# Optimization experiments

Hardware: AMD Instinct MI355X
Metric: run time of the kernel (lower is better)

Reference implementation:

```python
import jax, jax.numpy as jnp
import numpy as np

N = 8192
HID = 64
TAU = 0.8
LAMBDA = 0.5
POS_DENSITY = 0.005


def setup_inputs() -> dict:
    key = jax.random.key(0)
    k1, k2, k3, k4, k5, k6, k7 = jax.random.split(key, 7)
    x1 = jax.random.normal(k1, (N, HID), dtype=jnp.float32)
    x2 = jax.random.normal(k2, (N, HID), dtype=jnp.float32)
    # xavier_uniform with gain=1.414 for square [HID, HID] linears
    limit = 1.414 * np.sqrt(6.0 / (HID + HID))
    W1 = jax.random.uniform(k3, (HID, HID), dtype=jnp.float32, minval=-limit, maxval=limit)
    b1 = jnp.zeros((HID,), dtype=jnp.float32)
    W2 = jax.random.uniform(k4, (HID, HID), dtype=jnp.float32, minval=-limit, maxval=limit)
    b2 = jnp.zeros((HID,), dtype=jnp.float32)
    pm = (jax.random.uniform(k5, (N, N), dtype=jnp.float32) < POS_DENSITY).astype(jnp.float32)
    positive_matrix = jnp.maximum(pm, jnp.eye(N, dtype=jnp.float32))
    return {"x1": x1, "x2": x2, "W1": W1, "b1": b1, "W2": W2, "b2": b2,
            "positive_matrix": positive_matrix}


def _project(x, W1, b1, W2, b2):
    # nn.Linear(hidden, hidden) -> ELU -> nn.Linear(hidden, hidden)
    h = jax.nn.elu(x @ W1.T + b1)
    return h @ W2.T + b2


def _l2norm(z, eps=1e-12):
    # F.normalize(p=2, dim=1): x / max(||x||, eps)
    n = jnp.linalg.norm(z, axis=-1, keepdims=True)
    return z / jnp.maximum(n, eps)


def _sim(z1, z2, tau):
    return jnp.exp((_l2norm(z1) @ _l2norm(z2).T) / tau)  # [N, N]


def _masked_loss(sim_mat, pos):
    row = sim_mat / (jnp.sum(sim_mat, axis=-1, keepdims=True) + 1e-8)
    return -jnp.log(jnp.sum(row * pos, axis=-1) + 1e-8).mean()


def reference(x1, x2, W1, b1, W2, b2, positive_matrix):
    z1 = _project(x1, W1, b1, W2, b2)
    z2 = _project(x2, W1, b1, W2, b2)
    sc_mp = _sim(z1, z2, TAU)
    mp_sc = _sim(z2, z1, TAU)
    sc_loss = _masked_loss(sc_mp, positive_matrix)
    mp_loss = _masked_loss(mp_sc, positive_matrix)
    return sc_loss * LAMBDA + mp_loss * (1.0 - LAMBDA)
```

## Files before the change

### kernel.cpp

```cpp
#include <hip/hip_runtime.h>
#include <hip/hip_bf16.h>

#define N 8192
#define HID 64

typedef __attribute__((ext_vector_type(4))) float f32x4;
typedef __attribute__((ext_vector_type(8))) __bf16 bf16x8;

#if __has_builtin(__builtin_amdgcn_exp2f)
__device__ __forceinline__ float fast_exp2(float x) {
  return __builtin_amdgcn_exp2f(x);
}
#else
__device__ __forceinline__ float fast_exp2(float x) {
  float r;
  asm volatile("v_exp_f32 %0, %1" : "=v"(r) : "v"(x));
  return r;
}
#endif

__device__ __forceinline__ f32x4 nt_load4(const float* p) {
  return __builtin_nontemporal_load((const f32x4*)p);
}

__device__ __forceinline__ void gload_lds16(const void* g, float* l) {
  __builtin_amdgcn_global_load_lds(
      (const __attribute__((address_space(1))) void*)g,
      (__attribute__((address_space(3))) void*)l, 16, 0, 0);
}

__global__ __launch_bounds__(256) void proj_kernel(
    const float* __restrict__ x1, const float* __restrict__ x2,
    const float* __restrict__ W1, const float* __restrict__ b1,
    const float* __restrict__ W2, const float* __restrict__ b2,
    __bf16* __restrict__ Z1h, __bf16* __restrict__ Z2h)
{
  __shared__ __align__(16) float w1s[64*68];
  __shared__ __align__(16) float w2s[64*68];
  __shared__ __align__(16) float xs[4][64];
  __shared__ __align__(16) float hs[4][64];

  const int tid  = threadIdx.x;
  const int lane = tid & 63;
  const int w    = tid >> 6;

  for (int idx = tid; idx < 64*64; idx += 256) {
    int j = idx >> 6, k = idx & 63;
    w1s[j*68+k] = W1[idx];
    w2s[j*68+k] = W2[idx];
  }
  __syncthreads();

  const float bias1 = b1[lane];
  const float bias2 = b2[lane];

  const int wave_global = blockIdx.x * 4 + w;
  #pragma unroll 1
  for (int it = 0; it < 4; ++it) {
    int R = wave_global * 4 + it;
    const float* src; __bf16* dst;
    if (R < N) { src = x1 + (size_t)R*HID;      dst = Z1h + (size_t)R*HID; }
    else       { src = x2 + (size_t)(R-N)*HID;  dst = Z2h + (size_t)(R-N)*HID; }

    float xv = src[lane];
    xs[w][lane] = xv;
    float acc = bias1;
    #pragma unroll
    for (int qq = 0; qq < 16; ++qq) {
      f32x4 xq = *(const f32x4*)&xs[w][qq*4];
      f32x4 wq = *(const f32x4*)&w1s[lane*68 + qq*4];
      acc += xq.x*wq.x + xq.y*wq.y + xq.z*wq.z + xq.w*wq.w;
    }
    float h = acc > 0.f ? acc : expm1f(acc);
    hs[w][lane] = h;
    float acc2 = bias2;
    #pragma unroll
    for (int qq = 0; qq < 16; ++qq) {
      f32x4 hq = *(const f32x4*)&hs[w][qq*4];
      f32x4 wq = *(const f32x4*)&w2s[lane*68 + qq*4];
      acc2 += hq.x*wq.x + hq.y*wq.y + hq.z*wq.z + hq.w*wq.w;
    }
    float z = acc2;
    float ss = z*z;
    #pragma unroll
    for (int m = 1; m < 64; m <<= 1) ss += __shfl_xor(ss, m);
    float inv = 1.0f / fmaxf(sqrtf(ss), 1e-12f);
    dst[lane] = (__bf16)(z * inv);
  }
}

__global__ __launch_bounds__(256, 4) void sim_kernel(
    const __bf16* __restrict__ Z1h, const __bf16* __restrict__ Z2h,
    const float* __restrict__ pos,
    float* __restrict__ pr1, float* __restrict__ pn1,
    float* __restrict__ pr2, float* __restrict__ pn2)
{
  __shared__ __align__(16) float zs1[128*32];
  __shared__ __align__(16) float zs2[128*32];

  const int tid  = threadIdx.x;
  const int lane = tid & 63;
  const int w    = tid >> 6;
  const int r16  = lane & 15;
  const int q    = lane >> 4;

  const int jcid = blockIdx.x & 63;
  const int jb   = jcid * 128;
  const int ig   = (blockIdx.x >> 6) * 512;

  {
    const int r8 = lane >> 3;
    const int sl = (lane & 7) ^ r8;
    #pragma unroll
    for (int b = 0; b < 4; ++b) {
      const int row0 = w*32 + b*8;
      gload_lds16(Z1h + (size_t)(jb + row0 + r8)*HID + sl*8, &zs1[row0*32]);
      gload_lds16(Z2h + (size_t)(jb + row0 + r8)*HID + sl*8, &zs2[row0*32]);
    }
  }
  __syncthreads();

  const float Cexp = 1.8033688011112042f;

#define COMPC(S, PV) { \
    const int R  = (S)*16 + r16; \
    const int sw = r16 & 7; \
    bf16x8 b2lo = *(const bf16x8*)&zs2[R*32 + ((q    ) ^ sw)*4]; \
    bf16x8 b2hi = *(const bf16x8*)&zs2[R*32 + ((q + 4) ^ sw)*4]; \
    bf16x8 b1lo = *(const bf16x8*)&zs1[R*32 + ((q    ) ^ sw)*4]; \
    bf16x8 b1hi = *(const bf16x8*)&zs1[R*32 + ((q + 4) ^ sw)*4]; \
    f32x4 zero4 = {0.f,0.f,0.f,0.f}; \
    f32x4 d1 = __builtin_amdgcn_mfma_f32_16x16x32_bf16(b2lo, a1lo, zero4, 0,0,0); \
    d1       = __builtin_amdgcn_mfma_f32_16x16x32_bf16(b2hi, a1hi, d1,    0,0,0); \
    f32x4 d2 = __builtin_amdgcn_mfma_f32_16x16x32_bf16(b1lo, a2lo, zero4, 0,0,0); \
    d2       = __builtin_amdgcn_mfma_f32_16x16x32_bf16(b1hi, a2hi, d2,    0,0,0); \
    _Pragma("unroll") \
    for (int r = 0; r < 4; ++r) { \
      float e1 = fast_exp2(d1[r] * Cexp); \
      float e2 = fast_exp2(d2[r] * Cexp); \
      s1 += e1; n1 += e1 * PV[r]; \
      s2 += e2; n2 += e2 * PV[r]; \
    } }

  #pragma unroll 1
  for (int it = 0; it < 8; ++it) {
    const int i0 = ig + it*64 + w*16;

    const __bf16* z1r = Z1h + (size_t)(i0 + r16)*HID + q*8;
    const __bf16* z2r = Z2h + (size_t)(i0 + r16)*HID + q*8;
    const bf16x8 a1lo = *(const bf16x8*)(z1r);
    const bf16x8 a1hi = *(const bf16x8*)(z1r + 32);
    const bf16x8 a2lo = *(const bf16x8*)(z2r);
    const bf16x8 a2hi = *(const bf16x8*)(z2r + 32);

    const float* prow = pos + (size_t)(i0 + r16)*N + jb + q*4;
    const f32x4 P0 = nt_load4(prow);
    const f32x4 P1 = nt_load4(prow + 16);
    const f32x4 P2 = nt_load4(prow + 32);
    const f32x4 P3 = nt_load4(prow + 48);
    const f32x4 P4 = nt_load4(prow + 64);
    const f32x4 P5 = nt_load4(prow + 80);
    const f32x4 P6 = nt_load4(prow + 96);
    const f32x4 P7 = nt_load4(prow + 112);

    float s1 = 0.f, n1 = 0.f, s2 = 0.f, n2 = 0.f;

    COMPC(0, P0) COMPC(1, P1) COMPC(2, P2) COMPC(3, P3)
    COMPC(4, P4) COMPC(5, P5) COMPC(6, P6) COMPC(7, P7)

    s1 += __shfl_xor(s1, 16); s1 += __shfl_xor(s1, 32);
    n1 += __shfl_xor(n1, 16); n1 += __shfl_xor(n1, 32);
    s2 += __shfl_xor(s2, 16); s2 += __shfl_xor(s2, 32);
    n2 += __shfl_xor(n2, 16); n2 += __shfl_xor(n2, 32);

    if (lane < 16) {
      const size_t pidx = (size_t)jcid*N + i0 + r16;
      __builtin_nontemporal_store(s1, &pr1[pidx]);
      __builtin_nontemporal_store(n1, &pn1[pidx]);
      __builtin_nontemporal_store(s2, &pr2[pidx]);
      __builtin_nontemporal_store(n2, &pn2[pidx]);
    }
  }
#undef COMPC
}

__global__ __launch_bounds__(256) void loss_kernel(
    const float* __restrict__ pr1, const float* __restrict__ pn1,
    const float* __restrict__ pr2, const float* __restrict__ pn2,
    float* __restrict__ out)
{
  __shared__ float part[4];
  const int tid = threadIdx.x, lane = tid & 63, w = tid >> 6;
  const int row = blockIdx.x * 256 + tid;

  float rs1 = 0.f, nn1 = 0.f, rs2 = 0.f, nn2 = 0.f;
  #pragma unroll 4
  for (int jc = 0; jc < 64; ++jc) {
    rs1 += pr1[(size_t)jc*N + row];
    nn1 += pn1[(size_t)jc*N + row];
    rs2 += pr2[(size_t)jc*N + row];
    nn2 += pn2[(size_t)jc*N + row];
  }
  float sc = -logf(nn1/(rs1 + 1e-8f) + 1e-8f);
  float mp = -logf(nn2/(rs2 + 1e-8f) + 1e-8f);
  float acc = (0.5f*sc + 0.5f*mp) * (1.0f/N);

  #pragma unroll
  for (int m = 1; m < 64; m <<= 1) acc += __shfl_xor(acc, m);
  if (lane == 0) part[w] = acc;
  __syncthreads();
  if (tid == 0) atomicAdd(out, part[0] + part[1] + part[2] + part[3]);
}

extern "C" void kernel_launch(void* const* d_in, const int* in_sizes, int n_in,
                              void* d_out, int out_size, void* d_ws, size_t ws_size,
                              hipStream_t stream) {
  const float* x1  = (const float*)d_in[0];
  const float* x2  = (const float*)d_in[1];
  const float* W1  = (const float*)d_in[2];
  const float* b1  = (const float*)d_in[3];
  const float* W2  = (const float*)d_in[4];
  const float* b2  = (const float*)d_in[5];
  const float* pos = (const float*)d_in[6];

  char* ws = (char*)d_ws;
  __bf16* Z1h = (__bf16*)ws;
  __bf16* Z2h = (__bf16*)(ws + (size_t)N*HID*sizeof(__bf16));
  size_t zbytes = (size_t)2*N*HID*sizeof(__bf16);
  float* pr1 = (float*)(ws + zbytes);
  float* pn1 = pr1 + (size_t)64*N;
  float* pr2 = pn1 + (size_t)64*N;
  float* pn2 = pr2 + (size_t)64*N;

  proj_kernel<<<1024, 256, 0, stream>>>(x1, x2, W1, b1, W2, b2, Z1h, Z2h);
  sim_kernel<<<1024, 256, 0, stream>>>(Z1h, Z2h, pos, pr1, pn1, pr2, pn2);
  loss_kernel<<<32, 256, 0, stream>>>(pr1, pn1, pr2, pn2, (float*)d_out);
}
```

Baseline: 483.3 us.

## Widen sim_kernel column tiles and double-buffer positive-mask loads

Each sim block now covers 512 columns with 512 threads and stages four times more Z rows in LDS, which cuts the number of column chunks from 64 to 16. The grid drops from 1024 to 256 blocks. Inside each row strip, loads of the positive mask are double-buffered across four 128-column groups so HBM reads overlap the MFMA and exp work. The loss kernel reduces fewer partials. The costs are more registers and LDS per block and only 256 blocks, which may leave some CUs idle on a 256-CU part.

```diff
diff --git a/kernel.cpp b/kernel.cpp
--- a/kernel.cpp
+++ b/kernel.cpp
@@ -3,6 +3,7 @@
 
 #define N 8192
 #define HID 64
+#define NJC 16
 
 typedef __attribute__((ext_vector_type(4))) float f32x4;
 typedef __attribute__((ext_vector_type(8))) __bf16 bf16x8;
@@ -89,14 +90,14 @@
   }
 }
 
-__global__ __launch_bounds__(256, 4) void sim_kernel(
+__global__ __launch_bounds__(512, 2) void sim_kernel(
     const __bf16* __restrict__ Z1h, const __bf16* __restrict__ Z2h,
     const float* __restrict__ pos,
     float* __restrict__ pr1, float* __restrict__ pn1,
     float* __restrict__ pr2, float* __restrict__ pn2)
 {
-  __shared__ __align__(16) float zs1[128*32];
-  __shared__ __align__(16) float zs2[128*32];
+  __shared__ __align__(16) float zs1[512*32];
+  __shared__ __align__(16) float zs2[512*32];
 
   const int tid  = threadIdx.x;
   const int lane = tid & 63;
@@ -104,16 +105,16 @@
   const int r16  = lane & 15;
   const int q    = lane >> 4;
 
-  const int jcid = blockIdx.x & 63;
-  const int jb   = jcid * 128;
-  const int ig   = (blockIdx.x >> 6) * 512;
+  const int jcid = blockIdx.x & 15;
+  const int jb   = jcid * 512;
+  const int ig   = (blockIdx.x >> 4) * 512;
 
   {
     const int r8 = lane >> 3;
     const int sl = (lane & 7) ^ r8;
     #pragma unroll
-    for (int b = 0; b < 4; ++b) {
-      const int row0 = w*32 + b*8;
+    for (int b = 0; b < 8; ++b) {
+      const int row0 = w*64 + b*8;
       gload_lds16(Z1h + (size_t)(jb + row0 + r8)*HID + sl*8, &zs1[row0*32]);
       gload_lds16(Z2h + (size_t)(jb + row0 + r8)*HID + sl*8, &zs2[row0*32]);
     }
@@ -142,9 +143,22 @@
       s2 += e2; n2 += e2 * PV[r]; \
     } }
 
+#define LOADP(P, G) { \
+    const float* pg = prow + (G)*128; \
+    P##0 = nt_load4(pg);       P##1 = nt_load4(pg + 16); \
+    P##2 = nt_load4(pg + 32);  P##3 = nt_load4(pg + 48); \
+    P##4 = nt_load4(pg + 64);  P##5 = nt_load4(pg + 80); \
+    P##6 = nt_load4(pg + 96);  P##7 = nt_load4(pg + 112); \
+  }
+
+#define COMPG(G, P) { \
+    COMPC((G)*8+0, P##0) COMPC((G)*8+1, P##1) COMPC((G)*8+2, P##2) \
+    COMPC((G)*8+3, P##3) COMPC((G)*8+4, P##4) COMPC((G)*8+5, P##5) \
+    COMPC((G)*8+6, P##6) COMPC((G)*8+7, P##7) }
+
   #pragma unroll 1
-  for (int it = 0; it < 8; ++it) {
-    const int i0 = ig + it*64 + w*16;
+  for (int st = 0; st < 4; ++st) {
+    const int i0 = ig + w*64 + st*16;
 
     const __bf16* z1r = Z1h + (size_t)(i0 + r16)*HID + q*8;
     const __bf16* z2r = Z2h + (size_t)(i0 + r16)*HID + q*8;
@@ -154,19 +168,16 @@
     const bf16x8 a2hi = *(const bf16x8*)(z2r + 32);
 
     const float* prow = pos + (size_t)(i0 + r16)*N + jb + q*4;
-    const f32x4 P0 = nt_load4(prow);
-    const f32x4 P1 = nt_load4(prow + 16);
-    const f32x4 P2 = nt_load4(prow + 32);
-    const f32x4 P3 = nt_load4(prow + 48);
-    const f32x4 P4 = nt_load4(prow + 64);
-    const f32x4 P5 = nt_load4(prow + 80);
-    const f32x4 P6 = nt_load4(prow + 96);
-    const f32x4 P7 = nt_load4(prow + 112);
+    f32x4 PA0,PA1,PA2,PA3,PA4,PA5,PA6,PA7;
+    f32x4 PB0,PB1,PB2,PB3,PB4,PB5,PB6,PB7;
 
     float s1 = 0.f, n1 = 0.f, s2 = 0.f, n2 = 0.f;
 
-    COMPC(0, P0) COMPC(1, P1) COMPC(2, P2) COMPC(3, P3)
-    COMPC(4, P4) COMPC(5, P5) COMPC(6, P6) COMPC(7, P7)
+    LOADP(PA, 0)
+    LOADP(PB, 1)  COMPG(0, PA)
+    LOADP(PA, 2)  COMPG(1, PB)
+    LOADP(PB, 3)  COMPG(2, PA)
+    COMPG(3, PB)
 
     s1 += __shfl_xor(s1, 16); s1 += __shfl_xor(s1, 32);
     n1 += __shfl_xor(n1, 16); n1 += __shfl_xor(n1, 32);
@@ -182,6 +193,8 @@
     }
   }
 #undef COMPC
+#undef LOADP
+#undef COMPG
 }
 
 __global__ __launch_bounds__(256) void loss_kernel(
@@ -194,8 +207,8 @@
   const int row = blockIdx.x * 256 + tid;
 
   float rs1 = 0.f, nn1 = 0.f, rs2 = 0.f, nn2 = 0.f;
-  #pragma unroll 4
-  for (int jc = 0; jc < 64; ++jc) {
+  #pragma unroll
+  for (int jc = 0; jc < NJC; ++jc) {
     rs1 += pr1[(size_t)jc*N + row];
     nn1 += pn1[(size_t)jc*N + row];
     rs2 += pr2[(size_t)jc*N + row];
@@ -228,11 +241,11 @@
   __bf16* Z2h = (__bf16*)(ws + (size_t)N*HID*sizeof(__bf16));
   size_t zbytes = (size_t)2*N*HID*sizeof(__bf16);
   float* pr1 = (float*)(ws + zbytes);
-  float* pn1 = pr1 + (size_t)64*N;
-  float* pr2 = pn1 + (size_t)64*N;
-  float* pn2 = pr2 + (size_t)64*N;
+  float* pn1 = pr1 + (size_t)NJC*N;
+  float* pr2 = pn1 + (size_t)NJC*N;
+  float* pn2 = pr2 + (size_t)NJC*N;
 
   proj_kernel<<<1024, 256, 0, stream>>>(x1, x2, W1, b1, W2, b2, Z1h, Z2h);
-  sim_kernel<<<1024, 256, 0, stream>>>(Z1h, Z2h, pos, pr1, pn1, pr2, pn2);
+  sim_kernel<<<256, 512, 0, stream>>>(Z1h, Z2h, pos, pr1, pn1, pr2, pn2);
   loss_kernel<<<32, 256, 0, stream>>>(pr1, pn1, pr2, pn2, (float*)d_out);
 }
```

New measurement: 529.5 us. 1.1x slower.

## Pack positive mask into bitmask in a pre-pass before similarity kernel

Applied to the files above, without the earlier changes.

Adds a separate kernel that streams the dense float positive matrix once and packs it into 4-bit-per-byte masks. The similarity kernel then reads a compact mask and broadcasts it across lanes with shuffles, instead of issuing eight 16-byte nontemporal loads per row tile. The aim is to take the large strided mask stream out of the MFMA/exp loop, cutting its register use and load latency. The full matrix is still read every call, and the change adds a mask write, a mask read and one more launch.

```diff
diff --git a/kernel.cpp b/kernel.cpp
--- a/kernel.cpp
+++ b/kernel.cpp
@@ -3,6 +3,7 @@
 
 #define N 8192
 #define HID 64
+#define NJC 64
 
 typedef __attribute__((ext_vector_type(4))) float f32x4;
 typedef __attribute__((ext_vector_type(8))) __bf16 bf16x8;
@@ -19,14 +20,25 @@
 }
 #endif
 
-__device__ __forceinline__ f32x4 nt_load4(const float* p) {
-  return __builtin_nontemporal_load((const f32x4*)p);
-}
-
 __device__ __forceinline__ void gload_lds16(const void* g, float* l) {
   __builtin_amdgcn_global_load_lds(
       (const __attribute__((address_space(1))) void*)g,
       (__attribute__((address_space(3))) void*)l, 16, 0, 0);
+}
+
+__global__ __launch_bounds__(256) void mask_kernel(
+    const float* __restrict__ pos, unsigned char* __restrict__ mask)
+{
+  int idx = blockIdx.x * 256 + threadIdx.x;
+  const int stride = 2048 * 256;
+  #pragma unroll 1
+  for (int it = 0; it < 32; ++it) {
+    int i = idx + it * stride;
+    f32x4 v = *(const f32x4*)(pos + (size_t)i * 4);
+    unsigned b = (unsigned)(v.x != 0.f) | ((unsigned)(v.y != 0.f) << 1)
+               | ((unsigned)(v.z != 0.f) << 2) | ((unsigned)(v.w != 0.f) << 3);
+    mask[i] = (unsigned char)b;
+  }
 }
 
 __global__ __launch_bounds__(256) void proj_kernel(
@@ -91,7 +103,7 @@
 
 __global__ __launch_bounds__(256, 4) void sim_kernel(
     const __bf16* __restrict__ Z1h, const __bf16* __restrict__ Z2h,
-    const float* __restrict__ pos,
+    const unsigned char* __restrict__ mask,
     float* __restrict__ pr1, float* __restrict__ pn1,
     float* __restrict__ pr2, float* __restrict__ pn2)
 {
@@ -122,7 +134,7 @@
 
   const float Cexp = 1.8033688011112042f;
 
-#define COMPC(S, PV) { \
+#define COMPC(S, MK) { \
     const int R  = (S)*16 + r16; \
     const int sw = r16 & 7; \
     bf16x8 b2lo = *(const bf16x8*)&zs2[R*32 + ((q    ) ^ sw)*4]; \
@@ -138,8 +150,8 @@
     for (int r = 0; r < 4; ++r) { \
       float e1 = fast_exp2(d1[r] * Cexp); \
       float e2 = fast_exp2(d2[r] * Cexp); \
-      s1 += e1; n1 += e1 * PV[r]; \
-      s2 += e2; n2 += e2 * PV[r]; \
+      s1 += e1; s2 += e2; \
+      if (((MK) >> (8*q + r)) & 1u) { n1 += e1; n2 += e2; } \
     } }
 
   #pragma unroll 1
@@ -153,20 +165,23 @@
     const bf16x8 a2lo = *(const bf16x8*)(z2r);
     const bf16x8 a2hi = *(const bf16x8*)(z2r + 32);
 
-    const float* prow = pos + (size_t)(i0 + r16)*N + jb + q*4;
-    const f32x4 P0 = nt_load4(prow);
-    const f32x4 P1 = nt_load4(prow + 16);
-    const f32x4 P2 = nt_load4(prow + 32);
-    const f32x4 P3 = nt_load4(prow + 48);
-    const f32x4 P4 = nt_load4(prow + 64);
-    const f32x4 P5 = nt_load4(prow + 80);
-    const f32x4 P6 = nt_load4(prow + 96);
-    const f32x4 P7 = nt_load4(prow + 112);
+    const unsigned char* mrow = mask + (size_t)(i0 + r16)*(N/4) + jcid*32;
+    const unsigned W0 = *(const unsigned*)(mrow + 4*q);
+    const unsigned W1 = *(const unsigned*)(mrow + 16 + 4*q);
+
+    const unsigned M0 = __shfl((int)W0,      r16);
+    const unsigned M1 = __shfl((int)W0, 16 + r16);
+    const unsigned M2 = __shfl((int)W0, 32 + r16);
+    const unsigned M3 = __shfl((int)W0, 48 + r16);
+    const unsigned M4 = __shfl((int)W1,      r16);
+    const unsigned M5 = __shfl((int)W1, 16 + r16);
+    const unsigned M6 = __shfl((int)W1, 32 + r16);
+    const unsigned M7 = __shfl((int)W1, 48 + r16);
 
     float s1 = 0.f, n1 = 0.f, s2 = 0.f, n2 = 0.f;
 
-    COMPC(0, P0) COMPC(1, P1) COMPC(2, P2) COMPC(3, P3)
-    COMPC(4, P4) COMPC(5, P5) COMPC(6, P6) COMPC(7, P7)
+    COMPC(0, M0) COMPC(1, M1) COMPC(2, M2) COMPC(3, M3)
+    COMPC(4, M4) COMPC(5, M5) COMPC(6, M6) COMPC(7, M7)
 
     s1 += __shfl_xor(s1, 16); s1 += __shfl_xor(s1, 32);
     n1 += __shfl_xor(n1, 16); n1 += __shfl_xor(n1, 32);
@@ -195,7 +210,7 @@
 
   float rs1 = 0.f, nn1 = 0.f, rs2 = 0.f, nn2 = 0.f;
   #pragma unroll 4
-  for (int jc = 0; jc < 64; ++jc) {
+  for (int jc = 0; jc < NJC; ++jc) {
     rs1 += pr1[(size_t)jc*N + row];
     nn1 += pn1[(size_t)jc*N + row];
     rs2 += pr2[(size_t)jc*N + row];
@@ -228,11 +243,13 @@
   __bf16* Z2h = (__bf16*)(ws + (size_t)N*HID*sizeof(__bf16));
   size_t zbytes = (size_t)2*N*HID*sizeof(__bf16);
   float* pr1 = (float*)(ws + zbytes);
-  float* pn1 = pr1 + (size_t)64*N;
-  float* pr2 = pn1 + (size_t)64*N;
-  float* pn2 = pr2 + (size_t)64*N;
-
+  float* pn1 = pr1 + (size_t)NJC*N;
+  float* pr2 = pn1 + (size_t)NJC*N;
+  float* pn2 = pr2 + (size_t)NJC*N;
+  unsigned char* maskp = (unsigned char*)(pn2 + (size_t)NJC*N);
+
+  mask_kernel<<<2048, 256, 0, stream>>>(pos, maskp);
   proj_kernel<<<1024, 256, 0, stream>>>(x1, x2, W1, b1, W2, b2, Z1h, Z2h);
-  sim_kernel<<<1024, 256, 0, stream>>>(Z1h, Z2h, pos, pr1, pn1, pr2, pn2);
+  sim_kernel<<<1024, 256, 0, stream>>>(Z1h, Z2h, maskp, pr1, pn1, pr2, pn2);
   loss_kernel<<<32, 256, 0, stream>>>(pr1, pn1, pr2, pn2, (float*)d_out);
 }
```

Result: no change. 492.1 us (+1.8%).
